# Kernel tuning notes

Measured on AMD Instinct MI355X. Metric: run time of the kernel, lower is better.

The kernel has to match this reference:

```python
import jax, jax.numpy as jnp
import numpy as np

BS, SEQ, IN, H = 16, 1024, 512, 512


def setup_inputs() -> dict:
    key = jax.random.key(0)
    ks = jax.random.split(key, 10)
    std = 1.0 / np.sqrt(H)
    u = lambda k, shape: jax.random.uniform(k, shape, jnp.float32, -std, std)
    return {
        "x": jax.random.normal(ks[0], (BS, SEQ, IN), jnp.float32),
        # input projection fc: input_size -> hidden_size
        "Wfc": u(ks[1], (IN, H)),
        "bfc": u(ks[2], (H,)),
        # cell 1 (main hidden stream h): tree of matmuls + gated elementwise
        "W1x": u(ks[3], (2 * H, H)),  # layer-0 cells see duplicated features (2H)
        "W1h": u(ks[4], (H, H)),
        "W1g": u(ks[5], (H, H)),
        # cell 2 (second hidden stream c)
        "W2x": u(ks[6], (2 * H, H)),
        "W2h": u(ks[7], (H, H)),
        "W2g": u(ks[8], (H, H)),
    }


def reference(x, Wfc, bfc, W1x, W1h, W1g, W2x, W2h, W2g):
    bs = x.shape[0]
    # layer-0 input prep: fc projection then feature duplication (cat([x,x],dim=2))
    xp = x @ Wfc + bfc                      # [bs, seq, H]
    xp = jnp.concatenate([xp, xp], axis=-1)  # [bs, seq, 2H]
    xs = jnp.swapaxes(xp, 0, 1)             # [seq, bs, 2H] for scan over time

    h0 = jnp.zeros((bs, H), x.dtype)
    c0 = jnp.zeros((bs, H), x.dtype)

    def step(carry, x_t):
        h, c = carry  # hidden streams x2, x3 fed to each evolved cell
        h_new = jnp.tanh(x_t @ W1x + h @ W1h + jax.nn.sigmoid(c @ W1g) * h)
        c_new = jax.nn.sigmoid(x_t @ W2x + c @ W2h) * jnp.tanh(h @ W2g)
        return (h_new, c_new), h_new  # hidden_seq collects stream 0

    (h_fin, c_fin), hseq = jax.lax.scan(step, (h0, c0), xs)
    out = jnp.swapaxes(hseq, 0, 1)  # batch_first: [bs, seq, H]
    # final hidden states: [num_layers*(1), bs, H] per main stream
    return out, h_fin[None], c_fin[None]
```

## Files before the change

kernel.cpp:

```cpp
#include <hip/hip_runtime.h>


typedef unsigned short u16;
typedef unsigned int   u32;
typedef __attribute__((ext_vector_type(8))) short s8v;
typedef __attribute__((ext_vector_type(4))) float f4v;

__device__ __forceinline__ u16 f2bf_rne(float f){
  u32 u = __float_as_uint(f);
  u32 r = u + 0x7fffu + ((u >> 16) & 1u);
  return (u16)(r >> 16);
}
__device__ __forceinline__ float bf2f(u16 h){ return __uint_as_float(((u32)h) << 16); }
__device__ __forceinline__ f4v MFMA(s8v a, s8v b, f4v c){
  return __builtin_amdgcn_mfma_f32_16x16x32_bf16(a, b, c, 0, 0, 0);
}
__device__ __forceinline__ float sigmoidf_(float x){ return 1.0f / (1.0f + __expf(-x)); }
__device__ __forceinline__ float tanh_fast(float x){
  float e = __expf(2.0f * x);
  return 1.0f - 2.0f / (e + 1.0f);
}

template<bool CC> __device__ __forceinline__ s8v ld16(const u16* p){
  s8v r;
  if (CC) asm volatile("global_load_dwordx4 %0, %1, off sc0 sc1" : "=v"(r) : "v"(p));
  else    asm volatile("global_load_dwordx4 %0, %1, off"         : "=v"(r) : "v"(p));
  return r;
}
template<bool CC> __device__ __forceinline__ void st2(u16* p, u32 v){
  if (CC) asm volatile("global_store_short %0, %1, off sc0 sc1" :: "v"(p), "v"(v) : "memory");
  else    asm volatile("global_store_short %0, %1, off"         :: "v"(p), "v"(v) : "memory");
}
__device__ __forceinline__ void store_dword_cc(u32* p, u32 v){
  asm volatile("global_store_dword %0, %1, off sc0 sc1" :: "v"(p), "v"(v) : "memory");
}
__device__ __forceinline__ void store_dword_plain_wait(u32* p, u32 v){
  asm volatile("global_store_dword %0, %1, off\n\ts_waitcnt vmcnt(0)"
               :: "v"(p), "v"(v) : "memory");
}
__device__ __forceinline__ u32 load_dword_plain_wait(const u32* p){
  u32 r;
  asm volatile("global_load_dword %0, %1, off\n\ts_waitcnt vmcnt(0)"
               : "=v"(r) : "v"(p));
  return r;
}

#define SEQT 1024
#define NWG  16
#define PROT 16

static const size_t OFF_U1  = 0;
static const size_t OFF_U2  = 33554432;
static const size_t OFF_WCT = OFF_U2 + 16777216;
static const size_t OFF_ST  = OFF_WCT;
static const size_t OFF_WT  = OFF_WCT + 1048576;
static const size_t OFF_BC  = OFF_WT + 2097152;
static const size_t OFF_FL  = OFF_BC + 4096;
static const size_t OFF_TOK = OFF_FL + 65536;
static const size_t OFF_PRS = OFF_TOK + 4096;
static const size_t OFF_CTL = OFF_PRS + 4096;

__global__ void wcombk(const float* __restrict__ Wfc, const float* __restrict__ W1x,
                       const float* __restrict__ W2x, u16* __restrict__ Wct){
  __shared__ float A[16][17], B[16][17];
  const float* Wx = blockIdx.z ? W2x : W1x;
  int i0 = blockIdx.y * 16, n0 = blockIdx.x * 16;
  int tx = threadIdx.x, ty = threadIdx.y;
  float acc = 0.f;
  for (int kc = 0; kc < 512; kc += 16){
    A[ty][tx] = Wfc[(size_t)(i0 + ty) * 512 + kc + tx];
    B[ty][tx] = Wx[(size_t)(kc + ty) * 512 + n0 + tx]
              + Wx[(size_t)(kc + ty + 512) * 512 + n0 + tx];
    __syncthreads();
    #pragma unroll
    for (int kk = 0; kk < 16; ++kk) acc += A[ty][kk] * B[kk][tx];
    __syncthreads();
  }
  Wct[(size_t)(blockIdx.z * 512 + n0 + tx) * 512 + i0 + ty] = f2bf_rne(acc);
}

__global__ void bcombk(const float* __restrict__ bfc, const float* __restrict__ W1x,
                       const float* __restrict__ W2x, float* __restrict__ bc){
  int n = blockIdx.x * 256 + threadIdx.x;
  const float* Wx = (n < 512) ? W1x : W2x;
  int nl = n & 511;
  float acc = 0.f;
  for (int k = 0; k < 512; ++k)
    acc += bfc[k] * (Wx[(size_t)k * 512 + nl] + Wx[(size_t)(k + 512) * 512 + nl]);
  bc[n] = acc;
}

__global__ void wtk(const float* __restrict__ A, const float* __restrict__ B,
                    const float* __restrict__ C, const float* __restrict__ D,
                    u16* __restrict__ Wt){
  __shared__ float tile[32][33];
  const float* src = (blockIdx.z == 0) ? A : (blockIdx.z == 1) ? B
                    : (blockIdx.z == 2) ? C : D;
  int n0 = blockIdx.x * 32, k0 = blockIdx.y * 32;
  for (int i = threadIdx.y; i < 32; i += 8)
    tile[i][threadIdx.x] = src[(size_t)(k0 + i) * 512 + n0 + threadIdx.x];
  __syncthreads();
  for (int i = threadIdx.y; i < 32; i += 8)
    Wt[(size_t)blockIdx.z * 262144 + (size_t)(n0 + i) * 512 + k0 + threadIdx.x]
        = f2bf_rne(tile[threadIdx.x][i]);
}

__global__ __launch_bounds__(256) void gemmk(
    const float* __restrict__ x, const u16* __restrict__ Wct,
    const float* __restrict__ bc, float* __restrict__ U1, u16* __restrict__ U2){
  int l = threadIdx.x & 63, w = threadIdx.x >> 6;
  int lr = l & 15, lk = l >> 4;
  int m0 = blockIdx.y * 128 + (w & 1) * 64;
  int n0 = blockIdx.x * 64 + (w >> 1) * 32;
  f4v acc[4][2] = {};
  for (int ks = 0; ks < 16; ++ks){
    int k0 = ks * 32 + lk * 8;
    s8v bh0 = *(const s8v*)(Wct + (size_t)(n0 + lr) * 512 + k0);
    s8v bh1 = *(const s8v*)(Wct + (size_t)(n0 + 16 + lr) * 512 + k0);
    #pragma unroll
    for (int mi = 0; mi < 4; ++mi){
      const float* xp = x + (size_t)(m0 + mi * 16 + lr) * 512 + k0;
      f4v v0 = *(const f4v*)xp;
      f4v v1 = *(const f4v*)(xp + 4);
      s8v ah, al;
      #pragma unroll
      for (int j = 0; j < 4; ++j){
        { u32 u = __float_as_uint(v0[j]); ah[j] = (short)(u >> 16);
          float lof = v0[j] - __uint_as_float(u & 0xffff0000u);
          al[j] = (short)(__float_as_uint(lof) >> 16); }
        { u32 u = __float_as_uint(v1[j]); ah[j + 4] = (short)(u >> 16);
          float lof = v1[j] - __uint_as_float(u & 0xffff0000u);
          al[j + 4] = (short)(__float_as_uint(lof) >> 16); }
      }
      acc[mi][0] = MFMA(ah, bh0, acc[mi][0]);
      acc[mi][0] = MFMA(al, bh0, acc[mi][0]);
      acc[mi][1] = MFMA(ah, bh1, acc[mi][1]);
      acc[mi][1] = MFMA(al, bh1, acc[mi][1]);
    }
  }
  #pragma unroll
  for (int mi = 0; mi < 4; ++mi)
    #pragma unroll
    for (int ni = 0; ni < 2; ++ni){
      int n = n0 + ni * 16 + lr;
      float badd = bc[n];
      #pragma unroll
      for (int j = 0; j < 4; ++j){
        int r = m0 + mi * 16 + lk * 4 + j;
        int b = r >> 10, t = r & 1023;
        size_t oi = (size_t)(t * 16 + b) * 512;
        float v = acc[mi][ni][j] + badd;
        if (n < 512) U1[oi + n] = v;
        else         U2[oi + n - 512] = f2bf_rne(v);
      }
    }
}

template<bool CC>
__device__ __forceinline__ void scan_loop(
    int wg, int tid,
    const float* __restrict__ U1, const u16* __restrict__ U2,
    const u16* __restrict__ Wt, u16* __restrict__ st,
    u32* __restrict__ flags, float* __restrict__ out,
    float* xg, float* xt){
  const int w = tid >> 6, l = tid & 63;
  const int lr = l & 15, lk = l >> 4;
  const int ncol0 = wg * 32 + lr;

  s8v bf0[16], bf1[16];
  {
    const u16* Wm = Wt + (size_t)w * (512 * 512);
    #pragma unroll
    for (int ks = 0; ks < 16; ++ks){
      bf0[ks] = *(const s8v*)(Wm + (size_t)ncol0 * 512 + ks * 32 + lk * 8);
      bf1[ks] = *(const s8v*)(Wm + (size_t)(ncol0 + 16) * 512 + ks * 32 + lk * 8);
    }
  }
  const bool useH = (w == 0) || (w == 3);
  float hp0[4] = {0, 0, 0, 0}, hp1[4] = {0, 0, 0, 0};
  long guard = 0;

  for (int t = 0; t < SEQT; ++t){
    float uu0[4], uu1[4];
    if (w == 0){
      #pragma unroll
      for (int j = 0; j < 4; ++j){
        size_t ro = (size_t)(t * 16 + lk * 4 + j) * 512;
        uu0[j] = U1[ro + ncol0];
        uu1[j] = U1[ro + ncol0 + 16];
      }
    } else if (w == 2){
      #pragma unroll
      for (int j = 0; j < 4; ++j){
        size_t ro = (size_t)(t * 16 + lk * 4 + j) * 512;
        uu0[j] = bf2f(U2[ro + ncol0]);
        uu1[j] = bf2f(U2[ro + ncol0 + 16]);
      }
    }
    if (t > 0){
      const u32* fl = flags + (size_t)(t - 1) * NWG;
      for (;;){
        u32 v = 1u;
        if (l < NWG) v = __hip_atomic_load(fl + l, __ATOMIC_RELAXED, __HIP_MEMORY_SCOPE_AGENT);
        if (__all(v != 0u)) break;
        if (++guard > 1000000L) break;
      }
      __builtin_amdgcn_sched_barrier(0);
    }
    {
      u16* rb = st + (size_t)(t & (PROT - 1)) * 32768 + (useH ? 0 : 16384);
      u16* bhp = rb + lr * 512 + lk * 8;
      u16* blp = rb + 8192 + lr * 512 + lk * 8;
      s8v ah[16], al[16];
      #pragma unroll
      for (int ks = 0; ks < 16; ++ks){
        ah[ks] = ld16<CC>(bhp + ks * 32);
        al[ks] = ld16<CC>(blp + ks * 32);
      }
      asm volatile("s_waitcnt vmcnt(0)" ::: "memory");
      __builtin_amdgcn_sched_barrier(0);

      f4v a0 = {0, 0, 0, 0}, a1 = {0, 0, 0, 0};
      f4v b0 = {0, 0, 0, 0}, b1 = {0, 0, 0, 0};
      #pragma unroll
      for (int ks = 0; ks < 16; ++ks){
        a0 = MFMA(ah[ks], bf0[ks], a0);
        a1 = MFMA(ah[ks], bf1[ks], a1);
        b0 = MFMA(al[ks], bf0[ks], b0);
        b1 = MFMA(al[ks], bf1[ks], b1);
      }
      #pragma unroll
      for (int j = 0; j < 4; ++j){ a0[j] += b0[j]; a1[j] += b1[j]; }

      if (w == 1){
        #pragma unroll
        for (int j = 0; j < 4; ++j){
          xg[(0 * 16 + lk * 4 + j) * 16 + lr] = sigmoidf_(a0[j]);
          xg[(1 * 16 + lk * 4 + j) * 16 + lr] = sigmoidf_(a1[j]);
        }
      } else if (w == 3){
        #pragma unroll
        for (int j = 0; j < 4; ++j){
          xt[(0 * 16 + lk * 4 + j) * 16 + lr] = tanh_fast(a0[j]);
          xt[(1 * 16 + lk * 4 + j) * 16 + lr] = tanh_fast(a1[j]);
        }
      }
      __syncthreads();
      u16* wb = st + (size_t)((t + 1) & (PROT - 1)) * 32768;
      if (w == 0){
        #pragma unroll
        for (int j = 0; j < 4; ++j){
          int b = lk * 4 + j;
          float hn0 = tanh_fast(uu0[j] + a0[j] + xg[(0 * 16 + b) * 16 + lr] * hp0[j]);
          float hn1 = tanh_fast(uu1[j] + a1[j] + xg[(1 * 16 + b) * 16 + lr] * hp1[j]);
          hp0[j] = hn0; hp1[j] = hn1;
          size_t ob = (size_t)b * (SEQT * 512) + (size_t)t * 512;
          out[ob + ncol0]      = hn0;
          out[ob + ncol0 + 16] = hn1;
          u32 u0 = __float_as_uint(hn0), u1 = __float_as_uint(hn1);
          int bi = b * 512;
          st2<CC>(wb + bi + ncol0,      u0 >> 16);
          st2<CC>(wb + bi + ncol0 + 16, u1 >> 16);
          float lo0 = hn0 - __uint_as_float(u0 & 0xffff0000u);
          float lo1 = hn1 - __uint_as_float(u1 & 0xffff0000u);
          st2<CC>(wb + 8192 + bi + ncol0,      __float_as_uint(lo0) >> 16);
          st2<CC>(wb + 8192 + bi + ncol0 + 16, __float_as_uint(lo1) >> 16);
          if (t == SEQT - 1){
            out[8388608 + (size_t)b * 512 + ncol0]      = hn0;
            out[8388608 + (size_t)b * 512 + ncol0 + 16] = hn1;
          }
        }
      } else if (w == 2){
        #pragma unroll
        for (int j = 0; j < 4; ++j){
          int b = lk * 4 + j;
          float cn0 = sigmoidf_(uu0[j] + a0[j]) * xt[(0 * 16 + b) * 16 + lr];
          float cn1 = sigmoidf_(uu1[j] + a1[j]) * xt[(1 * 16 + b) * 16 + lr];
          u32 u0 = __float_as_uint(cn0), u1 = __float_as_uint(cn1);
          int bi = b * 512;
          st2<CC>(wb + 16384 + bi + ncol0,      u0 >> 16);
          st2<CC>(wb + 16384 + bi + ncol0 + 16, u1 >> 16);
          float lo0 = cn0 - __uint_as_float(u0 & 0xffff0000u);
          float lo1 = cn1 - __uint_as_float(u1 & 0xffff0000u);
          st2<CC>(wb + 24576 + bi + ncol0,      __float_as_uint(lo0) >> 16);
          st2<CC>(wb + 24576 + bi + ncol0 + 16, __float_as_uint(lo1) >> 16);
          if (t == SEQT - 1){
            out[8396800 + (size_t)b * 512 + ncol0]      = cn0;
            out[8396800 + (size_t)b * 512 + ncol0 + 16] = cn1;
          }
        }
      }
    }
    asm volatile("s_waitcnt vmcnt(0)" ::: "memory");
    __syncthreads();
    if (tid == 0) store_dword_cc(flags + (size_t)t * NWG + wg, 1u);
  }
}

__global__ __launch_bounds__(256, 1) void recurk(
    const float* __restrict__ U1, const u16* __restrict__ U2,
    const u16* __restrict__ Wt, u16* __restrict__ st,
    u32* __restrict__ flags, u32* __restrict__ tok, u32* __restrict__ prs,
    u32* __restrict__ ctl, float* __restrict__ out){
  const int tid = threadIdx.x;
  __shared__ int slot_sh, mode_sh;
  __shared__ float xg[2 * 16 * 16], xt[2 * 16 * 16];
  u32* cntp  = ctl;
  u32* modep = ctl + 16;

  if (tid == 0){
    int s = -1;
    u32 xcc;
    asm volatile("s_getreg_b32 %0, hwreg(HW_REG_XCC_ID)" : "=s"(xcc));
    if ((xcc & 0xfu) == 0u)
      s = (int)__hip_atomic_fetch_add(cntp, 1u, __ATOMIC_RELAXED,
                                      __HIP_MEMORY_SCOPE_AGENT);
    slot_sh = s;
  }
  __syncthreads();
  const int slot = slot_sh;

  if (tid == 0){
    if (slot >= 0 && slot < NWG){
      store_dword_plain_wait(tok + slot * 16, 0x5A5A0000u + (u32)slot);
      __hip_atomic_store(prs + slot * 16, 1u, __ATOMIC_RELAXED,
                         __HIP_MEMORY_SCOPE_AGENT);
    }
    if (blockIdx.x == 0){
      long g = 0;
      for (;;){
        u32 c = __hip_atomic_load(cntp, __ATOMIC_RELAXED, __HIP_MEMORY_SCOPE_AGENT);
        if (c >= NWG) break;
        if (++g > 2000000L){ atomicCAS(modep, 0u, 2u); break; }
      }
    }
    if (slot == 0){
      bool ok = true;
      long g = 0;
      for (int s2 = 1; s2 < NWG && ok; ++s2){
        for (;;){
          u32 p = __hip_atomic_load(prs + s2 * 16, __ATOMIC_RELAXED,
                                    __HIP_MEMORY_SCOPE_AGENT);
          if (p) break;
          if (++g > 5000000L){ ok = false; break; }
        }
      }
      if (ok){
        for (int s2 = 1; s2 < NWG; ++s2){
          u32 v = load_dword_plain_wait(tok + s2 * 16);
          if (v != 0x5A5A0000u + (u32)s2){ ok = false; break; }
        }
      }
      atomicCAS(modep, 0u, ok ? 1u : 3u);
    }
    long g = 0;
    u32 m;
    for (;;){
      m = __hip_atomic_load(modep, __ATOMIC_RELAXED, __HIP_MEMORY_SCOPE_AGENT);
      if (m) break;
      if (++g > 50000000L){ m = 3u; break; }
    }
    mode_sh = (int)m;
  }
  __syncthreads();
  const int mode = mode_sh;

  int wg; bool part;
  if (mode == 2){ wg = blockIdx.x; part = (wg < NWG); }
  else          { wg = slot;       part = (slot >= 0 && slot < NWG); }
  if (!part) return;

  if (mode == 1) scan_loop<false>(wg, tid, U1, U2, Wt, st, flags, out, xg, xt);
  else           scan_loop<true >(wg, tid, U1, U2, Wt, st, flags, out, xg, xt);
}

extern "C" void kernel_launch(void* const* d_in, const int* in_sizes, int n_in,
                              void* d_out, int out_size, void* d_ws, size_t ws_size,
                              hipStream_t stream){
  const float* x   = (const float*)d_in[0];
  const float* Wfc = (const float*)d_in[1];
  const float* bfc = (const float*)d_in[2];
  const float* W1x = (const float*)d_in[3];
  const float* W1h = (const float*)d_in[4];
  const float* W1g = (const float*)d_in[5];
  const float* W2x = (const float*)d_in[6];
  const float* W2h = (const float*)d_in[7];
  const float* W2g = (const float*)d_in[8];

  char* ws = (char*)d_ws;
  float* U1   = (float*)(ws + OFF_U1);
  u16*   U2   = (u16*)  (ws + OFF_U2);
  u16*   Wct  = (u16*)  (ws + OFF_WCT);
  u16*   st   = (u16*)  (ws + OFF_ST);
  u16*   Wt   = (u16*)  (ws + OFF_WT);
  float* bc   = (float*)(ws + OFF_BC);
  u32*   flags= (u32*)  (ws + OFF_FL);
  u32*   tok  = (u32*)  (ws + OFF_TOK);
  u32*   prs  = (u32*)  (ws + OFF_PRS);
  u32*   ctl  = (u32*)  (ws + OFF_CTL);
  float* out  = (float*)d_out;

  hipMemsetAsync(ws + OFF_FL, 0, 65536 + 4096 + 4096 + 4096, stream);

  wcombk<<<dim3(32, 32, 2), dim3(16, 16), 0, stream>>>(Wfc, W1x, W2x, Wct);
  bcombk<<<dim3(4), dim3(256), 0, stream>>>(bfc, W1x, W2x, bc);
  wtk   <<<dim3(16, 16, 4), dim3(32, 8), 0, stream>>>(W1h, W1g, W2h, W2g, Wt);
  gemmk <<<dim3(16, 128), dim3(256), 0, stream>>>(x, Wct, bc, U1, U2);
  hipMemsetAsync(ws + OFF_ST, 0, 1048576, stream);
  recurk<<<dim3(256), dim3(256), 0, stream>>>(U1, U2, Wt, st, flags, tok, prs, ctl, out);
}
```

Before: 6.680 ms.

## Use per-step atomic counters and prefetch next-step inputs in recurrent scan

In the same-XCC mode, the per-workgroup flag polling is replaced by a single per-step atomic counter. One lane of one wave spins on it with workgroup-scope atomics, then the block syncs. The U1/U2 inputs for the next timestep are prefetched during the current step, and the output-sequence stores are moved after the flag signal so they leave the critical path. The intent is to cut cross-workgroup barrier latency and global-load latency per timestep. The cost is a partial vmcnt wait and reliance on the memory-ordering assumptions of same-XCC atomics.

```diff
diff --git a/kernel.cpp b/kernel.cpp
--- a/kernel.cpp
+++ b/kernel.cpp
@@ -59,6 +59,7 @@
 static const size_t OFF_TOK = OFF_FL + 65536;
 static const size_t OFF_PRS = OFF_TOK + 4096;
 static const size_t OFF_CTL = OFF_PRS + 4096;
+static const size_t OFF_CN  = OFF_CTL + 4096;
 
 __global__ void wcombk(const float* __restrict__ Wfc, const float* __restrict__ W1x,
                        const float* __restrict__ W2x, u16* __restrict__ Wct){
@@ -161,8 +162,8 @@
     int wg, int tid,
     const float* __restrict__ U1, const u16* __restrict__ U2,
     const u16* __restrict__ Wt, u16* __restrict__ st,
-    u32* __restrict__ flags, float* __restrict__ out,
-    float* xg, float* xt){
+    u32* __restrict__ flags, u32* __restrict__ cnt,
+    float* __restrict__ out, float* xg, float* xt){
   const int w = tid >> 6, l = tid & 63;
   const int lr = l & 15, lk = l >> 4;
   const int ncol0 = wg * 32 + lr;
@@ -180,127 +181,186 @@
   float hp0[4] = {0, 0, 0, 0}, hp1[4] = {0, 0, 0, 0};
   long guard = 0;
 
+  float un0[4], un1[4], uc0[4], uc1[4];
+  u32   ur0[4], ur1[4];
+  if (w == 0){
+    #pragma unroll
+    for (int j = 0; j < 4; ++j){
+      size_t ro = (size_t)(lk * 4 + j) * 512;
+      un0[j] = U1[ro + ncol0];
+      un1[j] = U1[ro + ncol0 + 16];
+    }
+  } else if (w == 2){
+    #pragma unroll
+    for (int j = 0; j < 4; ++j){
+      size_t ro = (size_t)(lk * 4 + j) * 512;
+      ur0[j] = U2[ro + ncol0];
+      ur1[j] = U2[ro + ncol0 + 16];
+    }
+  }
+
   for (int t = 0; t < SEQT; ++t){
-    float uu0[4], uu1[4];
-    if (w == 0){
-      #pragma unroll
-      for (int j = 0; j < 4; ++j){
-        size_t ro = (size_t)(t * 16 + lk * 4 + j) * 512;
-        uu0[j] = U1[ro + ncol0];
-        uu1[j] = U1[ro + ncol0 + 16];
-      }
-    } else if (w == 2){
-      #pragma unroll
-      for (int j = 0; j < 4; ++j){
-        size_t ro = (size_t)(t * 16 + lk * 4 + j) * 512;
-        uu0[j] = bf2f(U2[ro + ncol0]);
-        uu1[j] = bf2f(U2[ro + ncol0 + 16]);
-      }
-    }
     if (t > 0){
-      const u32* fl = flags + (size_t)(t - 1) * NWG;
-      for (;;){
-        u32 v = 1u;
-        if (l < NWG) v = __hip_atomic_load(fl + l, __ATOMIC_RELAXED, __HIP_MEMORY_SCOPE_AGENT);
-        if (__all(v != 0u)) break;
-        if (++guard > 1000000L) break;
+      if (CC){
+        const u32* fl = flags + (size_t)(t - 1) * NWG;
+        for (;;){
+          u32 v = 1u;
+          if (l < NWG) v = __hip_atomic_load(fl + l, __ATOMIC_RELAXED, __HIP_MEMORY_SCOPE_AGENT);
+          if (__all(v != 0u)) break;
+          if (++guard > 1000000L) break;
+        }
+      } else {
+        if (w == 0){
+          for (;;){
+            u32 v = 0;
+            if (l == 0)
+              v = __hip_atomic_fetch_add(cnt + (t - 1), 0x10000u, __ATOMIC_RELAXED,
+                                         __HIP_MEMORY_SCOPE_WORKGROUP);
+            v = __builtin_amdgcn_readfirstlane(v);
+            if ((v & 0xffffu) >= NWG) break;
+            if (++guard > 8000000L) break;
+          }
+        }
+        __syncthreads();
       }
       __builtin_amdgcn_sched_barrier(0);
     }
+    u16* rb = st + (size_t)(t & (PROT - 1)) * 32768 + (useH ? 0 : 16384);
+    s8v ah[16], al[16];
     {
-      u16* rb = st + (size_t)(t & (PROT - 1)) * 32768 + (useH ? 0 : 16384);
       u16* bhp = rb + lr * 512 + lk * 8;
       u16* blp = rb + 8192 + lr * 512 + lk * 8;
-      s8v ah[16], al[16];
       #pragma unroll
       for (int ks = 0; ks < 16; ++ks){
         ah[ks] = ld16<CC>(bhp + ks * 32);
         al[ks] = ld16<CC>(blp + ks * 32);
       }
-      asm volatile("s_waitcnt vmcnt(0)" ::: "memory");
-      __builtin_amdgcn_sched_barrier(0);
-
-      f4v a0 = {0, 0, 0, 0}, a1 = {0, 0, 0, 0};
-      f4v b0 = {0, 0, 0, 0}, b1 = {0, 0, 0, 0};
-      #pragma unroll
-      for (int ks = 0; ks < 16; ++ks){
-        a0 = MFMA(ah[ks], bf0[ks], a0);
-        a1 = MFMA(ah[ks], bf1[ks], a1);
-        b0 = MFMA(al[ks], bf0[ks], b0);
-        b1 = MFMA(al[ks], bf1[ks], b1);
-      }
-      #pragma unroll
-      for (int j = 0; j < 4; ++j){ a0[j] += b0[j]; a1[j] += b1[j]; }
-
-      if (w == 1){
-        #pragma unroll
-        for (int j = 0; j < 4; ++j){
-          xg[(0 * 16 + lk * 4 + j) * 16 + lr] = sigmoidf_(a0[j]);
-          xg[(1 * 16 + lk * 4 + j) * 16 + lr] = sigmoidf_(a1[j]);
+    }
+    asm volatile("s_waitcnt vmcnt(0)" ::: "memory");
+    __builtin_amdgcn_sched_barrier(0);
+
+    if (w == 0){
+      #pragma unroll
+      for (int j = 0; j < 4; ++j){ uc0[j] = un0[j]; uc1[j] = un1[j]; }
+    } else if (w == 2){
+      #pragma unroll
+      for (int j = 0; j < 4; ++j){
+        uc0[j] = __uint_as_float(ur0[j] << 16);
+        uc1[j] = __uint_as_float(ur1[j] << 16);
+      }
+    }
+
+    f4v a0 = {0, 0, 0, 0}, a1 = {0, 0, 0, 0};
+    f4v b0 = {0, 0, 0, 0}, b1 = {0, 0, 0, 0};
+    #pragma unroll
+    for (int ks = 0; ks < 16; ++ks){
+      a0 = MFMA(ah[ks], bf0[ks], a0);
+      a1 = MFMA(ah[ks], bf1[ks], a1);
+      b0 = MFMA(al[ks], bf0[ks], b0);
+      b1 = MFMA(al[ks], bf1[ks], b1);
+    }
+    #pragma unroll
+    for (int j = 0; j < 4; ++j){ a0[j] += b0[j]; a1[j] += b1[j]; }
+
+    if (w == 1){
+      #pragma unroll
+      for (int j = 0; j < 4; ++j){
+        xg[(0 * 16 + lk * 4 + j) * 16 + lr] = sigmoidf_(a0[j]);
+        xg[(1 * 16 + lk * 4 + j) * 16 + lr] = sigmoidf_(a1[j]);
+      }
+    } else if (w == 3){
+      #pragma unroll
+      for (int j = 0; j < 4; ++j){
+        xt[(0 * 16 + lk * 4 + j) * 16 + lr] = tanh_fast(a0[j]);
+        xt[(1 * 16 + lk * 4 + j) * 16 + lr] = tanh_fast(a1[j]);
+      }
+    }
+    __syncthreads();
+    u16* wb = st + (size_t)((t + 1) & (PROT - 1)) * 32768;
+    const int tn = (t + 1 < SEQT) ? t + 1 : t;
+    float hn0v[4], hn1v[4], cn0v[4], cn1v[4];
+    if (w == 0){
+      #pragma unroll
+      for (int j = 0; j < 4; ++j){
+        int b = lk * 4 + j;
+        float hn0 = tanh_fast(uc0[j] + a0[j] + xg[(0 * 16 + b) * 16 + lr] * hp0[j]);
+        float hn1 = tanh_fast(uc1[j] + a1[j] + xg[(1 * 16 + b) * 16 + lr] * hp1[j]);
+        hp0[j] = hn0; hp1[j] = hn1;
+        hn0v[j] = hn0; hn1v[j] = hn1;
+        u32 u0 = __float_as_uint(hn0), u1 = __float_as_uint(hn1);
+        int bi = b * 512;
+        st2<CC>(wb + bi + ncol0,      u0 >> 16);
+        st2<CC>(wb + bi + ncol0 + 16, u1 >> 16);
+        float lo0 = hn0 - __uint_as_float(u0 & 0xffff0000u);
+        float lo1 = hn1 - __uint_as_float(u1 & 0xffff0000u);
+        st2<CC>(wb + 8192 + bi + ncol0,      __float_as_uint(lo0) >> 16);
+        st2<CC>(wb + 8192 + bi + ncol0 + 16, __float_as_uint(lo1) >> 16);
+      }
+      #pragma unroll
+      for (int j = 0; j < 4; ++j){
+        size_t ro = (size_t)(tn * 16 + lk * 4 + j) * 512;
+        un0[j] = U1[ro + ncol0];
+        un1[j] = U1[ro + ncol0 + 16];
+      }
+      asm volatile("s_waitcnt vmcnt(8)" ::: "memory");
+    } else if (w == 2){
+      #pragma unroll
+      for (int j = 0; j < 4; ++j){
+        int b = lk * 4 + j;
+        float cn0 = sigmoidf_(uc0[j] + a0[j]) * xt[(0 * 16 + b) * 16 + lr];
+        float cn1 = sigmoidf_(uc1[j] + a1[j]) * xt[(1 * 16 + b) * 16 + lr];
+        cn0v[j] = cn0; cn1v[j] = cn1;
+        u32 u0 = __float_as_uint(cn0), u1 = __float_as_uint(cn1);
+        int bi = b * 512;
+        st2<CC>(wb + 16384 + bi + ncol0,      u0 >> 16);
+        st2<CC>(wb + 16384 + bi + ncol0 + 16, u1 >> 16);
+        float lo0 = cn0 - __uint_as_float(u0 & 0xffff0000u);
+        float lo1 = cn1 - __uint_as_float(u1 & 0xffff0000u);
+        st2<CC>(wb + 24576 + bi + ncol0,      __float_as_uint(lo0) >> 16);
+        st2<CC>(wb + 24576 + bi + ncol0 + 16, __float_as_uint(lo1) >> 16);
+      }
+      #pragma unroll
+      for (int j = 0; j < 4; ++j){
+        size_t ro = (size_t)(tn * 16 + lk * 4 + j) * 512;
+        ur0[j] = U2[ro + ncol0];
+        ur1[j] = U2[ro + ncol0 + 16];
+      }
+      asm volatile("s_waitcnt vmcnt(8)" ::: "memory");
+    }
+    __syncthreads();
+    if (tid == 0){
+      if (CC) store_dword_cc(flags + (size_t)t * NWG + wg, 1u);
+      else    __hip_atomic_fetch_add(cnt + t, 1u, __ATOMIC_RELAXED,
+                                     __HIP_MEMORY_SCOPE_WORKGROUP);
+    }
+    if (w == 0){
+      #pragma unroll
+      for (int j = 0; j < 4; ++j){
+        int b = lk * 4 + j;
+        size_t ob = (size_t)b * (SEQT * 512) + (size_t)t * 512;
+        out[ob + ncol0]      = hn0v[j];
+        out[ob + ncol0 + 16] = hn1v[j];
+        if (t == SEQT - 1){
+          out[8388608 + (size_t)b * 512 + ncol0]      = hn0v[j];
+          out[8388608 + (size_t)b * 512 + ncol0 + 16] = hn1v[j];
         }
-      } else if (w == 3){
-        #pragma unroll
-        for (int j = 0; j < 4; ++j){
-          xt[(0 * 16 + lk * 4 + j) * 16 + lr] = tanh_fast(a0[j]);
-          xt[(1 * 16 + lk * 4 + j) * 16 + lr] = tanh_fast(a1[j]);
-        }
-      }
-      __syncthreads();
-      u16* wb = st + (size_t)((t + 1) & (PROT - 1)) * 32768;
-      if (w == 0){
-        #pragma unroll
-        for (int j = 0; j < 4; ++j){
-          int b = lk * 4 + j;
-          float hn0 = tanh_fast(uu0[j] + a0[j] + xg[(0 * 16 + b) * 16 + lr] * hp0[j]);
-          float hn1 = tanh_fast(uu1[j] + a1[j] + xg[(1 * 16 + b) * 16 + lr] * hp1[j]);
-          hp0[j] = hn0; hp1[j] = hn1;
-          size_t ob = (size_t)b * (SEQT * 512) + (size_t)t * 512;
-          out[ob + ncol0]      = hn0;
-          out[ob + ncol0 + 16] = hn1;
-          u32 u0 = __float_as_uint(hn0), u1 = __float_as_uint(hn1);
-          int bi = b * 512;
-          st2<CC>(wb + bi + ncol0,      u0 >> 16);
-          st2<CC>(wb + bi + ncol0 + 16, u1 >> 16);
-          float lo0 = hn0 - __uint_as_float(u0 & 0xffff0000u);
-          float lo1 = hn1 - __uint_as_float(u1 & 0xffff0000u);
-          st2<CC>(wb + 8192 + bi + ncol0,      __float_as_uint(lo0) >> 16);
-          st2<CC>(wb + 8192 + bi + ncol0 + 16, __float_as_uint(lo1) >> 16);
-          if (t == SEQT - 1){
-            out[8388608 + (size_t)b * 512 + ncol0]      = hn0;
-            out[8388608 + (size_t)b * 512 + ncol0 + 16] = hn1;
-          }
-        }
-      } else if (w == 2){
-        #pragma unroll
-        for (int j = 0; j < 4; ++j){
-          int b = lk * 4 + j;
-          float cn0 = sigmoidf_(uu0[j] + a0[j]) * xt[(0 * 16 + b) * 16 + lr];
-          float cn1 = sigmoidf_(uu1[j] + a1[j]) * xt[(1 * 16 + b) * 16 + lr];
-          u32 u0 = __float_as_uint(cn0), u1 = __float_as_uint(cn1);
-          int bi = b * 512;
-          st2<CC>(wb + 16384 + bi + ncol0,      u0 >> 16);
-          st2<CC>(wb + 16384 + bi + ncol0 + 16, u1 >> 16);
-          float lo0 = cn0 - __uint_as_float(u0 & 0xffff0000u);
-          float lo1 = cn1 - __uint_as_float(u1 & 0xffff0000u);
-          st2<CC>(wb + 24576 + bi + ncol0,      __float_as_uint(lo0) >> 16);
-          st2<CC>(wb + 24576 + bi + ncol0 + 16, __float_as_uint(lo1) >> 16);
-          if (t == SEQT - 1){
-            out[8396800 + (size_t)b * 512 + ncol0]      = cn0;
-            out[8396800 + (size_t)b * 512 + ncol0 + 16] = cn1;
-          }
-        }
-      }
-    }
-    asm volatile("s_waitcnt vmcnt(0)" ::: "memory");
-    __syncthreads();
-    if (tid == 0) store_dword_cc(flags + (size_t)t * NWG + wg, 1u);
+      }
+    } else if (w == 2 && t == SEQT - 1){
+      #pragma unroll
+      for (int j = 0; j < 4; ++j){
+        int b = lk * 4 + j;
+        out[8396800 + (size_t)b * 512 + ncol0]      = cn0v[j];
+        out[8396800 + (size_t)b * 512 + ncol0 + 16] = cn1v[j];
+      }
+    }
   }
 }
 
 __global__ __launch_bounds__(256, 1) void recurk(
     const float* __restrict__ U1, const u16* __restrict__ U2,
     const u16* __restrict__ Wt, u16* __restrict__ st,
-    u32* __restrict__ flags, u32* __restrict__ tok, u32* __restrict__ prs,
+    u32* __restrict__ flags, u32* __restrict__ cnt,
+    u32* __restrict__ tok, u32* __restrict__ prs,
     u32* __restrict__ ctl, float* __restrict__ out){
   const int tid = threadIdx.x;
   __shared__ int slot_sh, mode_sh;
@@ -370,8 +430,8 @@
   else          { wg = slot;       part = (slot >= 0 && slot < NWG); }
   if (!part) return;
 
-  if (mode == 1) scan_loop<false>(wg, tid, U1, U2, Wt, st, flags, out, xg, xt);
-  else           scan_loop<true >(wg, tid, U1, U2, Wt, st, flags, out, xg, xt);
+  if (mode == 1) scan_loop<false>(wg, tid, U1, U2, Wt, st, flags, cnt, out, xg, xt);
+  else           scan_loop<true >(wg, tid, U1, U2, Wt, st, flags, cnt, out, xg, xt);
 }
 
 extern "C" void kernel_launch(void* const* d_in, const int* in_sizes, int n_in,
@@ -398,14 +458,15 @@
   u32*   tok  = (u32*)  (ws + OFF_TOK);
   u32*   prs  = (u32*)  (ws + OFF_PRS);
   u32*   ctl  = (u32*)  (ws + OFF_CTL);
+  u32*   cnt  = (u32*)  (ws + OFF_CN);
   float* out  = (float*)d_out;
 
-  hipMemsetAsync(ws + OFF_FL, 0, 65536 + 4096 + 4096 + 4096, stream);
+  hipMemsetAsync(ws + OFF_FL, 0, 65536 + 4096 + 4096 + 4096 + 4096, stream);
 
   wcombk<<<dim3(32, 32, 2), dim3(16, 16), 0, stream>>>(Wfc, W1x, W2x, Wct);
   bcombk<<<dim3(4), dim3(256), 0, stream>>>(bfc, W1x, W2x, bc);
   wtk   <<<dim3(16, 16, 4), dim3(32, 8), 0, stream>>>(W1h, W1g, W2h, W2g, Wt);
   gemmk <<<dim3(16, 128), dim3(256), 0, stream>>>(x, Wct, bc, U1, U2);
   hipMemsetAsync(ws + OFF_ST, 0, 1048576, stream);
-  recurk<<<dim3(256), dim3(256), 0, stream>>>(U1, U2, Wt, st, flags, tok, prs, ctl, out);
-}
+  recurk<<<dim3(256), dim3(256), 0, stream>>>(U1, U2, Wt, st, flags, cnt, tok, prs, ctl, out);
+}
```

After: 6.445 ms. 3.5% less time.
